# Optimization experiments

Hardware: AMD Instinct MI355X
Metric: run time of the kernel (lower is better)

Reference implementation:

```python
import jax, jax.numpy as jnp
import numpy as np
from functools import partial

DT = 0.1
EPS_RES = 0.01
EIG_MIN = 0.1
EIG_CLIP = 0.99
CHUNK = 128

B, T, D, K = 8, 4096, 1024, 256


def setup_inputs() -> dict:
    key = jax.random.key(0)
    k1, k2, k3, k4, k5 = jax.random.split(key, 5)
    x = jax.random.normal(k1, (B, T, D), dtype=jnp.float32)
    # paper init: alpha ~ U(-3, 0)
    alpha_raw = -3.0 * jax.random.uniform(k2, (K,), dtype=jnp.float32)
    # omega_k = 2*pi*k/K
    omega = 2.0 * jnp.pi * jnp.arange(K, dtype=jnp.float32) / K
    W_in = jax.random.normal(k3, (K, D), dtype=jnp.float32) / np.sqrt(D)
    W_out = jax.random.normal(k4, (D, K), dtype=jnp.float32) / np.sqrt(K)
    M = jax.random.normal(k5, (K, K), dtype=jnp.float32)
    return {"x": x, "alpha_raw": alpha_raw, "omega": omega,
            "W_in": W_in, "W_out": W_out, "M": M}


def _forward(x, alpha_raw, omega, W_in, W_out, M):
    Bb, Tt, Dd = x.shape
    Kk = alpha_raw.shape[0]
    n_chunks = Tt // CHUNK

    # eigenvalue magnitude/phase with constraints
    mag = EIG_MIN + jax.nn.sigmoid(alpha_raw) * (EIG_CLIP - EIG_MIN)     # (K,)
    cos_p = jnp.cos(omega * DT)
    sin_p = jnp.sin(omega * DT)
    # resonance R = I + eps * M / ||M||_F
    R = jnp.eye(Kk, dtype=x.dtype) + EPS_RES * M / (jnp.linalg.norm(M) + 1e-8)

    # parallel input projection for all timesteps: (B,T,K)
    beta = jnp.einsum('btd,kd->btk', x, W_in)
    # (n_chunks, CHUNK, B, K) for scanning over chunks then timesteps
    beta_c = jnp.transpose(beta.reshape(Bb, n_chunks, CHUNK, Kk), (1, 2, 0, 3))

    def time_step(carry, b):
        r, i = carry                                     # (B,K) each
        nr = b + mag * (r * cos_p - i * sin_p)           # beta added to real only
        ni = mag * (r * sin_p + i * cos_p)
        return (nr, ni), (nr, ni)

    def chunk_step(carry, beta_ch):
        # beta_ch: (CHUNK, B, K)
        (_, _), (ar, ai) = jax.lax.scan(time_step, carry, beta_ch)
        # resonance coupling applied to every state of the chunk
        ar = ar @ R
        ai = ai @ R
        # state handed to next chunk is the resonance-coupled last state,
        # detached at the chunk boundary (as in the original training scheme)
        new_carry = (jax.lax.stop_gradient(ar[-1]), jax.lax.stop_gradient(ai[-1]))
        return new_carry, ar

    zero = jnp.zeros((Bb, Kk), dtype=x.dtype)
    _, states_real = jax.lax.scan(chunk_step, (zero, zero), beta_c)
    # states_real: (n_chunks, CHUNK, B, K) -> (B, T, K)
    states_real = jnp.transpose(states_real, (2, 0, 1, 3)).reshape(Bb, Tt, Kk)

    # parallel output projection (dropout is identity in eval)
    out = jnp.einsum('btk,dk->btd', states_real, W_out)
    return out


@jax.jit
def reference(x, alpha_raw, omega, W_in, W_out, M):
    return _forward(x, alpha_raw, omega, W_in, W_out, M)
```

## Files before the change

### kernel.cpp

```cpp
#include <hip/hip_runtime.h>
#include <math.h>


typedef __attribute__((ext_vector_type(8))) short short8;
typedef __attribute__((ext_vector_type(4))) float f32x4;

#define EPS_RES 0.01f

union U8 { unsigned u[4]; short8 s8; };

__device__ __forceinline__ unsigned short f2bf(float f) {
  unsigned u = __float_as_uint(f) + 0x8000u;
  return (unsigned short)(u >> 16);
}
__device__ __forceinline__ float bf2f(unsigned short h) {
  return __uint_as_float(((unsigned)h) << 16);
}
__device__ __forceinline__ unsigned pk2bf(float f0, float f1) {
  return __builtin_amdgcn_perm(__float_as_uint(f1) + 0x8000u,
                               __float_as_uint(f0) + 0x8000u, 0x07060302u);
}
__device__ __forceinline__ void gl_lds16(const void* g, void* l) {
  __builtin_amdgcn_global_load_lds(
      (const __attribute__((address_space(1))) unsigned*)g,
      (__attribute__((address_space(3))) unsigned*)l, 16, 0, 0);
}

__global__ __launch_bounds__(256) void k_setup(const float* __restrict__ M,
                                               float* __restrict__ part,
                                               const float* __restrict__ W,
                                               unsigned short* __restrict__ o) {
  const int bid = blockIdx.x;
  if (bid < 64) {
    const int i = (bid * 256 + threadIdx.x) * 4;
    const float4 v = *(const float4*)(M + i);
    float s = v.x * v.x + v.y * v.y + v.z * v.z + v.w * v.w;
    #pragma unroll
    for (int off = 32; off > 0; off >>= 1) s += __shfl_down(s, off);
    __shared__ float red[4];
    const int lane = threadIdx.x & 63, wv = threadIdx.x >> 6;
    if (lane == 0) red[wv] = s;
    __syncthreads();
    if (threadIdx.x == 0)
      part[bid] = red[0] + red[1] + red[2] + red[3];
  } else {
    const int i = ((bid - 64) * 256 + threadIdx.x) * 4;
    float4 v = *(const float4*)(W + i);
    uint2 p;
    p.x = pk2bf(v.x, v.y);
    p.y = pk2bf(v.z, v.w);
    *(uint2*)(o + i) = p;
  }
}

__device__ __forceinline__ float norm_scale(const float* __restrict__ part) {
  float nsum = 0.f;
  #pragma unroll
  for (int i = 0; i < 64; ++i) nsum += part[i];
  return EPS_RES / (sqrtf(nsum) + 1e-8f);
}

__global__ __launch_bounds__(256) void k_wcomb(const float* __restrict__ Wout,
                                               const float* __restrict__ Mm,
                                               const float* __restrict__ npart,
                                               unsigned short* __restrict__ WcT) {
  const int d0 = blockIdx.x * 8;
  const int k = threadIdx.x;
  __shared__ float wl[8][256];
  #pragma unroll
  for (int dd = 0; dd < 8; ++dd) wl[dd][k] = Wout[(size_t)(d0 + dd) * 256 + k];
  __syncthreads();
  float acc[8] = {0.f, 0.f, 0.f, 0.f, 0.f, 0.f, 0.f, 0.f};
  const float4* Mr = (const float4*)(Mm + (size_t)k * 256);
  for (int j4 = 0; j4 < 64; ++j4) {
    const float4 m4 = Mr[j4];
    #pragma unroll
    for (int dd = 0; dd < 8; ++dd) {
      acc[dd] = fmaf(m4.x, wl[dd][j4 * 4 + 0], acc[dd]);
      acc[dd] = fmaf(m4.y, wl[dd][j4 * 4 + 1], acc[dd]);
      acc[dd] = fmaf(m4.z, wl[dd][j4 * 4 + 2], acc[dd]);
      acc[dd] = fmaf(m4.w, wl[dd][j4 * 4 + 3], acc[dd]);
    }
  }
  const float s = norm_scale(npart);
  #pragma unroll
  for (int dd = 0; dd < 8; ++dd)
    WcT[(size_t)(d0 + dd) * 256 + k] =
        f2bf(Wout[(size_t)(d0 + dd) * 256 + k] + s * acc[dd]);
}

__global__ __launch_bounds__(256) void k_gemm1(const float* __restrict__ A,
                                               const unsigned short* __restrict__ Bw,
                                               float* __restrict__ C) {
  __shared__ __align__(16) float lA[2][64 * 64];
  const int tid = threadIdx.x;
  const int wv = tid >> 6, lane = tid & 63;
  const int m0 = blockIdx.x * 64;
  const int wn = wv;
  const int lrow = lane & 15, q = lane >> 4;

  const int s_r4 = lane >> 4;

  const unsigned short* Bt[4];
  #pragma unroll
  for (int t = 0; t < 4; ++t)
    Bt[t] = Bw + (size_t)(wn * 64 + t * 16 + lrow) * 1024 + q * 8;

  f32x4 acc[4][4] = {};

  auto stage = [&](int bf, int k0) {
    #pragma unroll
    for (int j = 0; j < 4; ++j) {
      const int rloc = j * 4 + s_r4;
      const int g = (lane & 15) ^ rloc;
      gl_lds16(A + (size_t)(m0 + wv * 16 + rloc) * 1024 + k0 + g * 4,
               &lA[bf][(wv * 16 + j * 4) * 64]);
    }
  };

  stage(0, 0);
  for (int s = 0; s < 16; ++s) {
    const int cur = s & 1;
    __syncthreads();
    if (s + 1 < 16) stage(cur ^ 1, (s + 1) * 64);

    #pragma unroll
    for (int ks = 0; ks < 2; ++ks) {
      short8 af[4], bfv[4];
      #pragma unroll
      for (int t = 0; t < 4; ++t) {
        const int ra = t * 16 + lrow;
        const int g0 = ks * 8 + 2 * q;
        const float4 lo =
            *(const float4*)&lA[cur][ra * 64 + ((g0 ^ (ra & 15)) << 2)];
        const float4 hi =
            *(const float4*)&lA[cur][ra * 64 + (((g0 + 1) ^ (ra & 15)) << 2)];
        U8 u;
        u.u[0] = pk2bf(lo.x, lo.y);
        u.u[1] = pk2bf(lo.z, lo.w);
        u.u[2] = pk2bf(hi.x, hi.y);
        u.u[3] = pk2bf(hi.z, hi.w);
        af[t] = u.s8;
        bfv[t] = *(const short8*)(Bt[t] + s * 64 + ks * 32);
      }
      #pragma unroll
      for (int tm = 0; tm < 4; ++tm)
        #pragma unroll
        for (int tn = 0; tn < 4; ++tn)
          acc[tm][tn] = __builtin_amdgcn_mfma_f32_16x16x32_bf16(
              af[tm], bfv[tn], acc[tm][tn], 0, 0, 0);
    }
  }

  const int rbase = m0 + q * 4;
  const int cbase = wn * 64 + lrow;
  #pragma unroll
  for (int tm = 0; tm < 4; ++tm)
    #pragma unroll
    for (int tn = 0; tn < 4; ++tn)
      #pragma unroll
      for (int r = 0; r < 4; ++r)
        C[(size_t)(rbase + tm * 16 + r) * 256 + (cbase + tn * 16)] =
            acc[tm][tn][r];
}

__global__ __launch_bounds__(256) void k_gemm2(const unsigned short* __restrict__ A,
                                               const unsigned short* __restrict__ Bw,
                                               float* __restrict__ C) {
  __shared__ __align__(16) unsigned short lA[2][128 * 64];
  const int tid = threadIdx.x;
  const int wv = tid >> 6, lane = tid & 63;
  const int bid = blockIdx.x + (blockIdx.y << 8);
  const int xcd = bid & 7, ii = bid >> 3;
  const int m0 = ((xcd << 5) + (ii >> 3)) * 128;
  const int n0 = (ii & 7) * 128;
  const int wm = wv & 1, wn = wv >> 1;
  const int lrow = lane & 15, q = lane >> 4;

  const int s_r8 = lane >> 3;

  const unsigned short* Bt[4];
  #pragma unroll
  for (int t = 0; t < 4; ++t)
    Bt[t] = Bw + (size_t)(n0 + wn * 64 + t * 16 + lrow) * 256 + q * 8;

  f32x4 acc[4][4] = {};

  auto stage = [&](int bf, int k0) {
    #pragma unroll
    for (int j = 0; j < 4; ++j) {
      const int rloc = j * 8 + s_r8;
      const int g = (lane & 7) ^ (rloc & 7);
      gl_lds16(A + (size_t)(m0 + wv * 32 + rloc) * 256 + k0 + g * 8,
               &lA[bf][(wv * 32 + j * 8) * 64]);
    }
  };

  stage(0, 0);
  for (int s = 0; s < 4; ++s) {
    const int cur = s & 1;
    __syncthreads();
    if (s + 1 < 4) stage(cur ^ 1, (s + 1) * 64);

    #pragma unroll
    for (int ks = 0; ks < 2; ++ks) {
      short8 af[4], bfv[4];
      #pragma unroll
      for (int t = 0; t < 4; ++t) {
        const int ra = wm * 64 + t * 16 + lrow;
        af[t] = *(const short8*)
            &lA[cur][ra * 64 + (((ks * 4 + q) ^ (ra & 7)) << 3)];
        bfv[t] = *(const short8*)(Bt[t] + s * 64 + ks * 32);
      }
      #pragma unroll
      for (int tm = 0; tm < 4; ++tm)
        #pragma unroll
        for (int tn = 0; tn < 4; ++tn)
          acc[tm][tn] = __builtin_amdgcn_mfma_f32_16x16x32_bf16(
              af[tm], bfv[tn], acc[tm][tn], 0, 0, 0);
    }
  }

  const int rbase = m0 + wm * 64 + (lane >> 4) * 4;
  const int cbase = n0 + wn * 64 + (lane & 15);
  #pragma unroll
  for (int tm = 0; tm < 4; ++tm)
    #pragma unroll
    for (int tn = 0; tn < 4; ++tn)
      #pragma unroll
      for (int r = 0; r < 4; ++r)
        C[(size_t)(rbase + tm * 16 + r) * 1024 + (cbase + tn * 16)] =
            acc[tm][tn][r];
}

__global__ __launch_bounds__(256) void k_scan(const float* __restrict__ beta,
                                              unsigned short* __restrict__ rez,
                                              float* __restrict__ lastR,
                                              float* __restrict__ lastI,
                                              const float* __restrict__ alpha_raw,
                                              const float* __restrict__ omega) {
  const int c = blockIdx.x & 31, b = blockIdx.x >> 5;
  const int k = threadIdx.x;
  const float a = alpha_raw[k];
  const float sig = 1.f / (1.f + expf(-a));
  const float mag = 0.1f + sig * (0.99f - 0.1f);
  const float om = omega[k] * 0.1f;
  const float lc = mag * cosf(om), ls = mag * sinf(om);

  const size_t m0 = (size_t)b * 4096 + (size_t)c * 128;
  const float* bp = beta + m0 * 256 + k;
  unsigned short* rp = rez + m0 * 256 + k;
  float r = 0.f, im = 0.f;
  #pragma unroll 8
  for (int t = 0; t < 128; ++t) {
    float be = bp[(size_t)t * 256];
    float nr = fmaf(lc, r, fmaf(-ls, im, be));
    float ni = fmaf(ls, r, lc * im);
    r = nr; im = ni;
    rp[(size_t)t * 256] = f2bf(r);
  }
  const int idx = (c * 8 + b) * 256 + k;
  lastR[idx] = r;
  lastI[idx] = im;
}

__global__ __launch_bounds__(256) void k_carry(const float* __restrict__ lastR,
                                               const float* __restrict__ lastI,
                                               const float* __restrict__ Mm,
                                               const float* __restrict__ npart,
                                               float* __restrict__ carR,
                                               float* __restrict__ carI) {
  const int c = blockIdx.x & 31, b = blockIdx.x >> 5;
  const int j = threadIdx.x;
  const int oidx = (c * 8 + b) * 256 + j;
  if (c == 0) {
    carR[oidx] = 0.f;
    carI[oidx] = 0.f;
    return;
  }
  __shared__ float lr[256], li[256];
  const int iidx = ((c - 1) * 8 + b) * 256;
  lr[j] = lastR[iidx + j];
  li[j] = lastI[iidx + j];
  __syncthreads();
  float ar = 0.f, ai = 0.f;
  for (int kk = 0; kk < 256; ++kk) {
    float m = Mm[(size_t)kk * 256 + j];
    ar = fmaf(lr[kk], m, ar);
    ai = fmaf(li[kk], m, ai);
  }
  const float s = norm_scale(npart);
  carR[oidx] = lr[j] + s * ar;
  carI[oidx] = li[j] + s * ai;
}

__global__ __launch_bounds__(256) void k_fixup(unsigned short* __restrict__ rez,
                                               const float* __restrict__ carR,
                                               const float* __restrict__ carI,
                                               const float* __restrict__ alpha_raw,
                                               const float* __restrict__ omega) {
  const int tg = blockIdx.x & 7;
  const int cb = blockIdx.x >> 3;
  const int b = cb & 7, c = (cb >> 3) + 1;
  const int k = threadIdx.x;
  const float a = alpha_raw[k];
  const float sig = 1.f / (1.f + expf(-a));
  const float mag = 0.1f + sig * (0.99f - 0.1f);
  const float om = omega[k] * 0.1f;
  const float l2m = log2f(mag);

  const float cr = carR[(c * 8 + b) * 256 + k];
  const float ci = carI[(c * 8 + b) * 256 + k];
  unsigned short* rp =
      rez + ((size_t)b * 4096 + (size_t)c * 128 + tg * 8) * 256 + k;
  #pragma unroll
  for (int tt = 0; tt < 8; ++tt) {
    const float tp1 = (float)(tg * 8 + tt + 1);
    const float p = exp2f(tp1 * l2m);
    const float ang = tp1 * om;
    const float hr = p * (cosf(ang) * cr - sinf(ang) * ci);
    rp[(size_t)tt * 256] = f2bf(bf2f(rp[(size_t)tt * 256]) + hr);
  }
}

extern "C" void kernel_launch(void* const* d_in, const int* in_sizes, int n_in,
                              void* d_out, int out_size, void* d_ws,
                              size_t ws_size, hipStream_t stream) {
  const float* x         = (const float*)d_in[0];
  const float* alpha_raw = (const float*)d_in[1];
  const float* omega     = (const float*)d_in[2];
  const float* W_in      = (const float*)d_in[3];
  const float* W_out     = (const float*)d_in[4];
  const float* Mm        = (const float*)d_in[5];
  float* out = (float*)d_out;

  char* ws = (char*)d_ws;
  float*          beta  = (float*)(ws);
  unsigned short* rez   = (unsigned short*)(ws + 33554432);
  float*          lastR = (float*)(ws + 50331648);
  float*          lastI = (float*)(ws + 50331648 + 262144);
  float*          carR  = (float*)(ws + 50331648 + 2 * 262144);
  float*          carI  = (float*)(ws + 50331648 + 3 * 262144);
  unsigned short* WcT   = (unsigned short*)(ws + 50331648 + 4 * 262144);
  float*          npart = (float*)(ws + 50331648 + 4 * 262144 + 524288);
  unsigned short* WinT  = (unsigned short*)d_out;

  k_setup<<<320, 256, 0, stream>>>(Mm, npart, W_in, WinT);
  k_wcomb<<<128, 256, 0, stream>>>(W_out, Mm, npart, WcT);
  k_gemm1<<<512, 256, 0, stream>>>(x, WinT, beta);
  k_scan<<<256, 256, 0, stream>>>(beta, rez, lastR, lastI, alpha_raw, omega);
  k_carry<<<256, 256, 0, stream>>>(lastR, lastI, Mm, npart, carR, carI);
  k_fixup<<<1984, 256, 0, stream>>>(rez, carR, carI, alpha_raw, omega);
  k_gemm2<<<dim3(256, 8), 256, 0, stream>>>(rez, WcT, out);
}
```

Measured before the change: 334.5 us.

## Use single-wave GEMM blocks with triple-buffered async LDS loads and no barriers

Both projection GEMMs move from 256-thread blocks to 64-thread single-wavefront blocks with smaller tiles (32x64 and 64x64). A three-stage LDS ring is filled by direct global-to-LDS loads and gated with explicit vmcnt waits instead of __syncthreads, so loads for step s+2 overlap compute on step s. Grids grow to 4096 and 8192 blocks with XCD-aware block remapping. The goal is better latency hiding and occupancy without workgroup barriers, at the cost of less B-operand reuse per block and more redundant weight reads.

```diff
diff --git a/kernel.cpp b/kernel.cpp
--- a/kernel.cpp
+++ b/kernel.cpp
@@ -89,147 +89,139 @@
         f2bf(Wout[(size_t)(d0 + dd) * 256 + k] + s * acc[dd]);
 }
 
-__global__ __launch_bounds__(256) void k_gemm1(const float* __restrict__ A,
-                                               const unsigned short* __restrict__ Bw,
-                                               float* __restrict__ C) {
-  __shared__ __align__(16) float lA[2][64 * 64];
-  const int tid = threadIdx.x;
-  const int wv = tid >> 6, lane = tid & 63;
-  const int m0 = blockIdx.x * 64;
-  const int wn = wv;
+__global__ __launch_bounds__(64) void k_gemm1(const float* __restrict__ A,
+                                              const unsigned short* __restrict__ Bw,
+                                              float* __restrict__ C) {
+  __shared__ __align__(16) float lA[3][32 * 32];
+  const int lane = threadIdx.x;
+  const int wg = ((blockIdx.x & 7) << 9) + (blockIdx.x >> 3);
+  const int m0 = (wg >> 2) * 32;
+  const int n0 = (wg & 3) * 64;
   const int lrow = lane & 15, q = lane >> 4;
 
-  const int s_r4 = lane >> 4;
+  const int s_r8 = lane >> 3;
+  const int s_g = (lane & 7) ^ s_r8;
 
   const unsigned short* Bt[4];
   #pragma unroll
   for (int t = 0; t < 4; ++t)
-    Bt[t] = Bw + (size_t)(wn * 64 + t * 16 + lrow) * 1024 + q * 8;
-
-  f32x4 acc[4][4] = {};
+    Bt[t] = Bw + (size_t)(n0 + t * 16 + lrow) * 1024 + q * 8;
+
+  f32x4 acc[2][4] = {};
 
   auto stage = [&](int bf, int k0) {
     #pragma unroll
-    for (int j = 0; j < 4; ++j) {
-      const int rloc = j * 4 + s_r4;
-      const int g = (lane & 15) ^ rloc;
-      gl_lds16(A + (size_t)(m0 + wv * 16 + rloc) * 1024 + k0 + g * 4,
-               &lA[bf][(wv * 16 + j * 4) * 64]);
+    for (int j = 0; j < 4; ++j)
+      gl_lds16(A + (size_t)(m0 + j * 8 + s_r8) * 1024 + k0 + s_g * 4,
+               &lA[bf][(j * 8) * 32]);
+  };
+
+  auto compute = [&](int cur, int s) {
+    short8 bfv[4];
+    #pragma unroll
+    for (int tn = 0; tn < 4; ++tn)
+      bfv[tn] = *(const short8*)(Bt[tn] + s * 32);
+    short8 af[2];
+    #pragma unroll
+    for (int tm = 0; tm < 2; ++tm) {
+      const int ra = tm * 16 + lrow, sw = ra & 7;
+      const float4 lo = *(const float4*)&lA[cur][ra * 32 + (((2 * q) ^ sw) << 2)];
+      const float4 hi = *(const float4*)&lA[cur][ra * 32 + (((2 * q + 1) ^ sw) << 2)];
+      U8 u;
+      u.u[0] = pk2bf(lo.x, lo.y);
+      u.u[1] = pk2bf(lo.z, lo.w);
+      u.u[2] = pk2bf(hi.x, hi.y);
+      u.u[3] = pk2bf(hi.z, hi.w);
+      af[tm] = u.s8;
     }
+    #pragma unroll
+    for (int tm = 0; tm < 2; ++tm)
+      #pragma unroll
+      for (int tn = 0; tn < 4; ++tn)
+        acc[tm][tn] = __builtin_amdgcn_mfma_f32_16x16x32_bf16(
+            af[tm], bfv[tn], acc[tm][tn], 0, 0, 0);
   };
 
   stage(0, 0);
-  for (int s = 0; s < 16; ++s) {
-    const int cur = s & 1;
-    __syncthreads();
-    if (s + 1 < 16) stage(cur ^ 1, (s + 1) * 64);
-
-    #pragma unroll
-    for (int ks = 0; ks < 2; ++ks) {
-      short8 af[4], bfv[4];
-      #pragma unroll
-      for (int t = 0; t < 4; ++t) {
-        const int ra = t * 16 + lrow;
-        const int g0 = ks * 8 + 2 * q;
-        const float4 lo =
-            *(const float4*)&lA[cur][ra * 64 + ((g0 ^ (ra & 15)) << 2)];
-        const float4 hi =
-            *(const float4*)&lA[cur][ra * 64 + (((g0 + 1) ^ (ra & 15)) << 2)];
-        U8 u;
-        u.u[0] = pk2bf(lo.x, lo.y);
-        u.u[1] = pk2bf(lo.z, lo.w);
-        u.u[2] = pk2bf(hi.x, hi.y);
-        u.u[3] = pk2bf(hi.z, hi.w);
-        af[t] = u.s8;
-        bfv[t] = *(const short8*)(Bt[t] + s * 64 + ks * 32);
-      }
-      #pragma unroll
-      for (int tm = 0; tm < 4; ++tm)
-        #pragma unroll
-        for (int tn = 0; tn < 4; ++tn)
-          acc[tm][tn] = __builtin_amdgcn_mfma_f32_16x16x32_bf16(
-              af[tm], bfv[tn], acc[tm][tn], 0, 0, 0);
-    }
-  }
-
-  const int rbase = m0 + q * 4;
-  const int cbase = wn * 64 + lrow;
-  #pragma unroll
-  for (int tm = 0; tm < 4; ++tm)
+  stage(1, 32);
+  for (int s = 0; s < 31; ++s) {
+    asm volatile("s_waitcnt vmcnt(4)" ::: "memory");
+    if (s + 2 < 32) stage((s + 2) % 3, (s + 2) * 32);
+    compute(s % 3, s);
+  }
+  asm volatile("s_waitcnt vmcnt(0)" ::: "memory");
+  compute(31 % 3, 31);
+
+  #pragma unroll
+  for (int tm = 0; tm < 2; ++tm)
     #pragma unroll
     for (int tn = 0; tn < 4; ++tn)
       #pragma unroll
       for (int r = 0; r < 4; ++r)
-        C[(size_t)(rbase + tm * 16 + r) * 256 + (cbase + tn * 16)] =
+        C[(size_t)(m0 + tm * 16 + q * 4 + r) * 256 + (n0 + tn * 16 + lrow)] =
             acc[tm][tn][r];
 }
 
-__global__ __launch_bounds__(256) void k_gemm2(const unsigned short* __restrict__ A,
-                                               const unsigned short* __restrict__ Bw,
-                                               float* __restrict__ C) {
-  __shared__ __align__(16) unsigned short lA[2][128 * 64];
-  const int tid = threadIdx.x;
-  const int wv = tid >> 6, lane = tid & 63;
-  const int bid = blockIdx.x + (blockIdx.y << 8);
-  const int xcd = bid & 7, ii = bid >> 3;
-  const int m0 = ((xcd << 5) + (ii >> 3)) * 128;
-  const int n0 = (ii & 7) * 128;
-  const int wm = wv & 1, wn = wv >> 1;
+__global__ __launch_bounds__(64) void k_gemm2(const unsigned short* __restrict__ A,
+                                              const unsigned short* __restrict__ Bw,
+                                              float* __restrict__ C) {
+  __shared__ __align__(16) unsigned short lA[3][64 * 32];
+  const int lane = threadIdx.x;
+  const int wg = ((blockIdx.x & 7) << 10) + (blockIdx.x >> 3);
+  const int m0 = (wg >> 4) * 64;
+  const int n0 = (wg & 15) * 64;
   const int lrow = lane & 15, q = lane >> 4;
 
-  const int s_r8 = lane >> 3;
+  const int s_r16 = lane >> 2;
+  const int s_g = (lane & 3) ^ ((s_r16 >> 1) & 3);
 
   const unsigned short* Bt[4];
   #pragma unroll
   for (int t = 0; t < 4; ++t)
-    Bt[t] = Bw + (size_t)(n0 + wn * 64 + t * 16 + lrow) * 256 + q * 8;
+    Bt[t] = Bw + (size_t)(n0 + t * 16 + lrow) * 256 + q * 8;
 
   f32x4 acc[4][4] = {};
 
   auto stage = [&](int bf, int k0) {
     #pragma unroll
-    for (int j = 0; j < 4; ++j) {
-      const int rloc = j * 8 + s_r8;
-      const int g = (lane & 7) ^ (rloc & 7);
-      gl_lds16(A + (size_t)(m0 + wv * 32 + rloc) * 256 + k0 + g * 8,
-               &lA[bf][(wv * 32 + j * 8) * 64]);
+    for (int j = 0; j < 4; ++j)
+      gl_lds16(A + (size_t)(m0 + j * 16 + s_r16) * 256 + k0 + s_g * 8,
+               &lA[bf][(j * 16) * 32]);
+  };
+
+  auto compute = [&](int cur, int s) {
+    short8 af[4], bfv[4];
+    #pragma unroll
+    for (int t = 0; t < 4; ++t) {
+      bfv[t] = *(const short8*)(Bt[t] + s * 32);
+      const int ra = t * 16 + lrow;
+      af[t] = *(const short8*)&lA[cur][ra * 32 + ((q ^ ((ra >> 1) & 3)) << 3)];
     }
+    #pragma unroll
+    for (int tm = 0; tm < 4; ++tm)
+      #pragma unroll
+      for (int tn = 0; tn < 4; ++tn)
+        acc[tm][tn] = __builtin_amdgcn_mfma_f32_16x16x32_bf16(
+            af[tm], bfv[tn], acc[tm][tn], 0, 0, 0);
   };
 
   stage(0, 0);
-  for (int s = 0; s < 4; ++s) {
-    const int cur = s & 1;
-    __syncthreads();
-    if (s + 1 < 4) stage(cur ^ 1, (s + 1) * 64);
-
-    #pragma unroll
-    for (int ks = 0; ks < 2; ++ks) {
-      short8 af[4], bfv[4];
-      #pragma unroll
-      for (int t = 0; t < 4; ++t) {
-        const int ra = wm * 64 + t * 16 + lrow;
-        af[t] = *(const short8*)
-            &lA[cur][ra * 64 + (((ks * 4 + q) ^ (ra & 7)) << 3)];
-        bfv[t] = *(const short8*)(Bt[t] + s * 64 + ks * 32);
-      }
-      #pragma unroll
-      for (int tm = 0; tm < 4; ++tm)
-        #pragma unroll
-        for (int tn = 0; tn < 4; ++tn)
-          acc[tm][tn] = __builtin_amdgcn_mfma_f32_16x16x32_bf16(
-              af[tm], bfv[tn], acc[tm][tn], 0, 0, 0);
-    }
-  }
-
-  const int rbase = m0 + wm * 64 + (lane >> 4) * 4;
-  const int cbase = n0 + wn * 64 + (lane & 15);
+  stage(1, 32);
+  for (int s = 0; s < 7; ++s) {
+    asm volatile("s_waitcnt vmcnt(4)" ::: "memory");
+    if (s + 2 < 8) stage((s + 2) % 3, (s + 2) * 32);
+    compute(s % 3, s);
+  }
+  asm volatile("s_waitcnt vmcnt(0)" ::: "memory");
+  compute(7 % 3, 7);
+
   #pragma unroll
   for (int tm = 0; tm < 4; ++tm)
     #pragma unroll
     for (int tn = 0; tn < 4; ++tn)
       #pragma unroll
       for (int r = 0; r < 4; ++r)
-        C[(size_t)(rbase + tm * 16 + r) * 1024 + (cbase + tn * 16)] =
+        C[(size_t)(m0 + tm * 16 + q * 4 + r) * 1024 + (n0 + tn * 16 + lrow)] =
             acc[tm][tn][r];
 }
 
@@ -347,9 +339,9 @@
 
   k_setup<<<320, 256, 0, stream>>>(Mm, npart, W_in, WinT);
   k_wcomb<<<128, 256, 0, stream>>>(W_out, Mm, npart, WcT);
-  k_gemm1<<<512, 256, 0, stream>>>(x, WinT, beta);
+  k_gemm1<<<4096, 64, 0, stream>>>(x, WinT, beta);
   k_scan<<<256, 256, 0, stream>>>(beta, rez, lastR, lastI, alpha_raw, omega);
   k_carry<<<256, 256, 0, stream>>>(lastR, lastI, Mm, npart, carR, carI);
   k_fixup<<<1984, 256, 0, stream>>>(rez, carR, carI, alpha_raw, omega);
-  k_gemm2<<<dim3(256, 8), 256, 0, stream>>>(rez, WcT, out);
-}
+  k_gemm2<<<8192, 64, 0, stream>>>(rez, WcT, out);
+}
```

After: 392.6 us. +17.4%, slower.
